# Kernel tuning notes

Hardware: AMD Instinct MI355X
Metric: run time of the kernel (lower is better)

The kernel has to match this reference:

```python
import jax, jax.numpy as jnp
import numpy as np

B, T, D, H = 2, 2048, 2048, 16
HD = D // H  # head_dim = 128
NEG = -1e9


def setup_inputs() -> dict:
    key = jax.random.key(0)
    k1, k2, k3 = jax.random.split(key, 3)
    x = jax.random.normal(k1, (B, T, D), dtype=jnp.float32)
    # additive causal mask: 0 on/below diagonal, large negative above
    mask = jnp.where(jnp.tril(jnp.ones((T, T), dtype=bool)), 0.0, NEG).astype(jnp.float32)
    causal_mask = mask[None, None]  # [1,1,T,T]
    w_qkv = jax.random.normal(k2, (3 * D, D), dtype=jnp.float32) * (D ** -0.5)
    w_out = jax.random.normal(k3, (D, D), dtype=jnp.float32) * (D ** -0.5)
    b_out = jnp.zeros((D,), dtype=jnp.float32)
    return {"x": x, "causal_mask": causal_mask, "w_qkv": w_qkv, "w_out": w_out, "b_out": b_out}


def reference(x, causal_mask, w_qkv, w_out, b_out):
    scale = HD ** -0.5
    qkv = jnp.einsum('btd,ed->bte', x, w_qkv)          # [B,T,3D]
    q, k, v = jnp.split(qkv, 3, axis=-1)
    def heads(t):  # [B,T,D] -> [B,H,T,HD]
        return t.reshape(B, T, H, HD).transpose(0, 2, 1, 3)
    q, k, v = heads(q), heads(k), heads(v)
    attn = jnp.einsum('bhqd,bhkd->bhqk', q, k) * scale + causal_mask
    attn = jax.nn.softmax(attn, axis=-1)
    out = jnp.einsum('bhqk,bhkd->bhqd', attn, v)       # [B,H,T,HD]
    out = out.transpose(0, 2, 1, 3).reshape(B, T, D)
    return jnp.einsum('btd,ed->bte', out, w_out) + b_out
```

## Files before the change

kernel.cpp:

```cpp
#include <hip/hip_runtime.h>
#include <stdint.h>

typedef uint16_t u16;
typedef __attribute__((ext_vector_type(8))) short short8;
typedef __attribute__((ext_vector_type(4))) float f32x4;
typedef __attribute__((ext_vector_type(16))) float f32x16;

#define MFMA16(a, b, c) __builtin_amdgcn_mfma_f32_16x16x32_bf16((a), (b), (c), 0, 0, 0)
#define MFMA32(a, b, c) __builtin_amdgcn_mfma_f32_32x32x16_bf16((a), (b), (c), 0, 0, 0)
#define AS1 __attribute__((address_space(1)))
#define AS3 __attribute__((address_space(3)))

__device__ __forceinline__ void gld_lds16(const u16* g, u16* l) {
  __builtin_amdgcn_global_load_lds((const AS1 void*)g, (AS3 void*)l, 16, 0, 0);
}

__device__ __forceinline__ u16 f2bf(float f) {
  uint32_t u = __float_as_uint(f);
  u += 0x7fffu + ((u >> 16) & 1u);
  return (u16)(u >> 16);
}

__global__ __launch_bounds__(256) void cvt_all(const float* __restrict__ x,
                                               const float* __restrict__ wqkv,
                                               const float* __restrict__ wout,
                                               u16* __restrict__ xb,
                                               u16* __restrict__ wqkvb,
                                               u16* __restrict__ woutb) {
  const int n1 = 8388608 / 4, n2 = 12582912 / 4;
  int i = blockIdx.x * 256 + threadIdx.x;
  const float* src;
  u16* dst;
  int j;
  if (i < n1) {
    src = x; dst = xb; j = i;
  } else if (i < n1 + n2) {
    src = wqkv; dst = wqkvb; j = i - n1;
  } else {
    src = wout; dst = woutb; j = i - n1 - n2;
  }
  float4 v = ((const float4*)src)[j];
  uint2 o;
  o.x = (uint32_t)f2bf(v.x) | ((uint32_t)f2bf(v.y) << 16);
  o.y = (uint32_t)f2bf(v.z) | ((uint32_t)f2bf(v.w) << 16);
  ((uint2*)dst)[j] = o;
}

__device__ __forceinline__ void gemm_core(const u16* __restrict__ Ab,
                                          const u16* __restrict__ Bb,
                                          int K, int lda, int ldb, u16* As,
                                          u16* Bs, int tid, f32x4 acc[4][4]) {
  const int lane = tid & 63, w = tid >> 6;
  const int wr = w >> 1, wc = w & 1;
  const int lo = lane & 15, q4 = lane >> 4;
  for (int k0 = 0; k0 < K; k0 += 64) {
#pragma unroll
    for (int s = 0; s < 4; ++s) {
      const int c = tid + s * 256;
      const int row = c >> 3, cc = c & 7;
      const int cs = cc ^ (row & 7);
      gld_lds16(Ab + (size_t)row * lda + k0 + cs * 8, As + c * 8);
      gld_lds16(Bb + (size_t)row * ldb + k0 + cs * 8, Bs + c * 8);
    }
    __syncthreads();
#pragma unroll
    for (int kk = 0; kk < 2; ++kk) {
      short8 af[4], bf[4];
#pragma unroll
      for (int i = 0; i < 4; ++i) {
        const int r = wr * 64 + i * 16 + lo;
        const int ch = (kk * 4 + q4) ^ (r & 7);
        af[i] = *(const short8*)(As + r * 64 + ch * 8);
      }
#pragma unroll
      for (int i = 0; i < 4; ++i) {
        const int r = wc * 64 + i * 16 + lo;
        const int ch = (kk * 4 + q4) ^ (r & 7);
        bf[i] = *(const short8*)(Bs + r * 64 + ch * 8);
      }
#pragma unroll
      for (int i = 0; i < 4; ++i)
#pragma unroll
        for (int j = 0; j < 4; ++j) acc[i][j] = MFMA16(af[i], bf[j], acc[i][j]);
    }
    __syncthreads();
  }
}

__global__ __launch_bounds__(256) void proj_gemm(const u16* __restrict__ xb,
                                                 const u16* __restrict__ wqkvb,
                                                 u16* __restrict__ qkb,
                                                 u16* __restrict__ vtb) {
  __shared__ u16 As[128 * 64];
  __shared__ u16 Bs[128 * 64];
  const int bx = blockIdx.x, tid = threadIdx.x;
  const u16 *Ab, *Bb;
  u16* C;
  if (bx < 1024) {
    const int mt = bx >> 5, nt = bx & 31;
    Ab = xb + (size_t)mt * 128 * 2048;
    Bb = wqkvb + (size_t)nt * 128 * 2048;
    C = qkb + (size_t)mt * 128 * 4096 + nt * 128;
  } else {
    const int idx = bx - 1024, mt = idx >> 5, nt = idx & 31;
    Ab = wqkvb + (size_t)(4096 + mt * 128) * 2048;
    Bb = xb + (size_t)nt * 128 * 2048;
    C = vtb + (size_t)mt * 128 * 4096 + nt * 128;
  }
  f32x4 acc[4][4];
  const f32x4 fzero = {0.f, 0.f, 0.f, 0.f};
#pragma unroll
  for (int i = 0; i < 4; ++i)
#pragma unroll
    for (int j = 0; j < 4; ++j) acc[i][j] = fzero;

  gemm_core(Ab, Bb, 2048, 2048, 2048, As, Bs, tid, acc);

  const int lane = tid & 63, w = tid >> 6;
  const int wr = w >> 1, wc = w & 1;
  const int lo = lane & 15, q4 = lane >> 4;
#pragma unroll
  for (int i = 0; i < 4; ++i)
#pragma unroll
    for (int j = 0; j < 4; ++j) {
      const int col = wc * 64 + j * 16 + lo;
#pragma unroll
      for (int e = 0; e < 4; ++e) {
        const int row = wr * 64 + i * 16 + q4 * 4 + e;
        C[(size_t)row * 4096 + col] = f2bf(acc[i][j][e]);
      }
    }
}

__global__ __launch_bounds__(256) void out_gemm(const u16* __restrict__ A,
                                                const u16* __restrict__ B,
                                                float* __restrict__ Cf,
                                                const float* __restrict__ bias) {
  __shared__ u16 As[128 * 64];
  __shared__ u16 Bs[128 * 64];
  const int bx = blockIdx.x, tid = threadIdx.x;
  const int mt = bx >> 4, nt = bx & 15;
  const u16* Ab = A + (size_t)mt * 128 * 2048;
  const u16* Bb = B + (size_t)nt * 128 * 2048;
  f32x4 acc[4][4];
  const f32x4 fzero = {0.f, 0.f, 0.f, 0.f};
#pragma unroll
  for (int i = 0; i < 4; ++i)
#pragma unroll
    for (int j = 0; j < 4; ++j) acc[i][j] = fzero;

  gemm_core(Ab, Bb, 2048, 2048, 2048, As, Bs, tid, acc);

  const int lane = tid & 63, w = tid >> 6;
  const int wr = w >> 1, wc = w & 1;
  const int lo = lane & 15, q4 = lane >> 4;
#pragma unroll
  for (int i = 0; i < 4; ++i)
#pragma unroll
    for (int j = 0; j < 4; ++j) {
      const int col = nt * 128 + wc * 64 + j * 16 + lo;
      const float bv = bias[col];
#pragma unroll
      for (int e = 0; e < 4; ++e) {
        const int row = mt * 128 + wr * 64 + i * 16 + q4 * 4 + e;
        Cf[(size_t)row * 2048 + col] = acc[i][j][e] + bv;
      }
    }
}

__device__ __forceinline__ int swz(int r, int c) {
  return r * 128 + (c ^ (((r ^ (r >> 3)) & 7) << 4));
}

__global__ __launch_bounds__(512) void flash_attn(const u16* __restrict__ qk,
                                                  const u16* __restrict__ vt,
                                                  u16* __restrict__ aout) {
  constexpr int T = 2048, WQK = 4096, D = 2048;
  constexpr int TILE = 128 * 128;
  __shared__ u16 smem[5 * TILE];

  const int bx = blockIdx.x;
  const int p = bx >> 5;
  const int g = bx & 31;
  const int h = g & 15, b = g >> 4;
  const int tid = threadIdx.x, lane = tid & 63, w = tid >> 6;
  const int wr = w >> 1, wcc = w & 1;
  const int l31 = lane & 31, h5 = lane >> 5;

  const u16* Qb = qk + (size_t)b * T * WQK + h * 128;
  const u16* Kb = Qb + 2048;
  const u16* Vtb = vt + (size_t)h * 128 * 4096 + b * 2048;
  u16* Ps = smem + 4 * TILE;

  const float cexp = 0.08838834764831843f * 1.4426950408889634f;
  short8 onesf;
#pragma unroll
  for (int j = 0; j < 8; ++j) onesf[j] = (short)0x3F80;

  for (int half = 0; half < 2; ++half) {
    const int qt = half ? p : 15 - p;
    const int q0 = qt * 128;

    short8 qf[8];
#pragma unroll
    for (int kc = 0; kc < 8; ++kc)
      qf[kc] = *(const short8*)(Qb + (size_t)(q0 + wr * 32 + l31) * WQK +
                                kc * 16 + h5 * 8);

    f32x16 o[2], osum;
#pragma unroll
    for (int e = 0; e < 16; ++e) { o[0][e] = 0.f; o[1][e] = 0.f; osum[e] = 0.f; }

    __syncthreads();
#pragma unroll
    for (int s = 0; s < 4; ++s) {
      const int c = tid + s * 512, r = c >> 4, cc = c & 15;
      const int cs = cc ^ (((r ^ (r >> 3)) & 7) << 1);
      gld_lds16(Kb + (size_t)r * WQK + cs * 8, smem + c * 8);
      gld_lds16(Vtb + (size_t)r * 4096 + cs * 8, smem + 2 * TILE + c * 8);
    }

    for (int kt = 0; kt <= qt; ++kt) {
      const int curo = (kt & 1) * TILE, nxto = TILE - curo;
      __syncthreads();
      if (kt < qt) {
        const int k0n = (kt + 1) * 128;
#pragma unroll
        for (int s = 0; s < 4; ++s) {
          const int c = tid + s * 512, r = c >> 4, cc = c & 15;
          const int cs = cc ^ (((r ^ (r >> 3)) & 7) << 1);
          gld_lds16(Kb + (size_t)(k0n + r) * WQK + cs * 8, smem + nxto + c * 8);
          gld_lds16(Vtb + (size_t)r * 4096 + k0n + cs * 8,
                    smem + 2 * TILE + nxto + c * 8);
        }
      }

      const u16* Ksc = smem + curo;
      const u16* Vsc = smem + 2 * TILE + curo;

      f32x16 s2[2];
#pragma unroll
      for (int e = 0; e < 16; ++e) { s2[0][e] = 0.f; s2[1][e] = 0.f; }
#pragma unroll
      for (int kc = 0; kc < 8; ++kc)
#pragma unroll
        for (int ct = 0; ct < 2; ++ct) {
          short8 kf = *(const short8*)&Ksc[swz(wcc * 64 + ct * 32 + l31,
                                               kc * 16 + h5 * 8)];
          s2[ct] = MFMA32(qf[kc], kf, s2[ct]);
        }

      const bool diag = (kt == qt);
#pragma unroll
      for (int ct = 0; ct < 2; ++ct) {
        const int kcol = wcc * 64 + ct * 32 + l31;
#pragma unroll
        for (int reg = 0; reg < 16; ++reg) {
          const int qrow = wr * 32 + (reg & 3) + 8 * (reg >> 2) + 4 * h5;
          float pv = exp2f(s2[ct][reg] * cexp);
          if (diag && (kcol > qrow)) pv = 0.f;
          Ps[swz(qrow, kcol)] = f2bf(pv);
        }
      }
      asm volatile("s_waitcnt lgkmcnt(0)\n\ts_barrier" ::: "memory");

#pragma unroll
      for (int kc = 0; kc < 8; ++kc) {
        short8 pa = *(const short8*)&Ps[swz(wr * 32 + l31, kc * 16 + h5 * 8)];
        osum = MFMA32(pa, onesf, osum);
#pragma unroll
        for (int dt = 0; dt < 2; ++dt) {
          short8 vf = *(const short8*)&Vsc[swz(wcc * 64 + dt * 32 + l31,
                                               kc * 16 + h5 * 8)];
          o[dt] = MFMA32(pa, vf, o[dt]);
        }
      }
    }

#pragma unroll
    for (int reg = 0; reg < 16; ++reg) {
      const int row = q0 + wr * 32 + (reg & 3) + 8 * (reg >> 2) + 4 * h5;
      const float inv = 1.f / osum[reg];
#pragma unroll
      for (int dt = 0; dt < 2; ++dt)
        aout[(size_t)(b * T + row) * D + h * 128 + wcc * 64 + dt * 32 + l31] =
            f2bf(o[dt][reg] * inv);
    }
  }
}

extern "C" void kernel_launch(void* const* d_in, const int* in_sizes, int n_in,
                              void* d_out, int out_size, void* d_ws, size_t ws_size,
                              hipStream_t stream) {
  const float* x = (const float*)d_in[0];
  const float* w_qkv = (const float*)d_in[2];
  const float* w_out = (const float*)d_in[3];
  const float* b_out = (const float*)d_in[4];
  float* out = (float*)d_out;

  const int BT = 4096, D = 2048, D3 = 6144;
  u16* xb = (u16*)d_ws;
  u16* wqkvb = xb + (size_t)BT * D;
  u16* woutb = wqkvb + (size_t)D3 * D;
  u16* qkb = woutb + (size_t)D * D;
  u16* vtb = qkb + (size_t)BT * 4096;
  u16* attnb = vtb + (size_t)D * BT;

  const int total4 = (BT * D + D3 * D + D * D) / 4;
  cvt_all<<<total4 / 256, 256, 0, stream>>>(x, w_qkv, w_out, xb, wqkvb, woutb);
  proj_gemm<<<1536, 256, 0, stream>>>(xb, wqkvb, qkb, vtb);
  flash_attn<<<256, 512, 0, stream>>>(qkb, vtb, attnb);
  out_gemm<<<512, 256, 0, stream>>>(attnb, woutb, out, b_out);
}
```

Measured before the change: 363.6 us.

## Triple-buffer GEMM K-loop with 256-row proj tiles and XCD-aware block remap

Replaces the single-buffered, two-barrier GEMM loop with a 3-stage LDS ring over K=32 slices. Each stage is issued two iterations ahead and guarded by one vmcnt-wait plus barrier, so global-to-LDS loads overlap the MFMAs. The projection GEMM moves to 256x128 tiles with 8 MFMA rows per wave, halving the grid, and both GEMMs remap block IDs so neighbouring tiles land on the same XCD for L2 reuse. The swizzle changes to a rotation, and MFMA sections are wrapped with s_setprio. The trade is more registers and LDS per block, which limits occupancy to 2 blocks per CU, plus more barriers per unit of work from the smaller K step.

```diff
diff --git a/kernel.cpp b/kernel.cpp
--- a/kernel.cpp
+++ b/kernel.cpp
@@ -46,99 +46,133 @@
   ((uint2*)dst)[j] = o;
 }
 
-__device__ __forceinline__ void gemm_core(const u16* __restrict__ Ab,
-                                          const u16* __restrict__ Bb,
-                                          int K, int lda, int ldb, u16* As,
-                                          u16* Bs, int tid, f32x4 acc[4][4]) {
+template <int N>
+__device__ __forceinline__ void bar_vm() {
+  asm volatile("s_waitcnt vmcnt(%0)\n\ts_barrier" ::"n"(N) : "memory");
+}
+
+template <int MFR>
+__device__ __forceinline__ void gemm_core3(const u16* __restrict__ Ab,
+                                           const u16* __restrict__ Bb,
+                                           u16* sm, int tid,
+                                           f32x4 acc[MFR][4]) {
+  constexpr int AROWS = MFR * 32;
+  constexpr int ASZ = AROWS * 32;
+  constexpr int BSZ = 128 * 32;
+  constexpr int BUF = ASZ + BSZ;
+  constexpr int NT = 64;
+  constexpr int ALD = AROWS / 64;
+  constexpr int VN = ALD + 2;
   const int lane = tid & 63, w = tid >> 6;
   const int wr = w >> 1, wc = w & 1;
   const int lo = lane & 15, q4 = lane >> 4;
-  for (int k0 = 0; k0 < K; k0 += 64) {
-#pragma unroll
-    for (int s = 0; s < 4; ++s) {
+  const int ch = (q4 + 4 - (lo >> 2)) & 3;
+
+  auto stage = [&](int g) {
+    u16* As = sm + (g % 3) * BUF;
+    u16* Bs = As + ASZ;
+    const int k0 = g * 32;
+#pragma unroll
+    for (int s = 0; s < ALD; ++s) {
       const int c = tid + s * 256;
-      const int row = c >> 3, cc = c & 7;
-      const int cs = cc ^ (row & 7);
-      gld_lds16(Ab + (size_t)row * lda + k0 + cs * 8, As + c * 8);
-      gld_lds16(Bb + (size_t)row * ldb + k0 + cs * 8, Bs + c * 8);
-    }
-    __syncthreads();
-#pragma unroll
-    for (int kk = 0; kk < 2; ++kk) {
-      short8 af[4], bf[4];
-#pragma unroll
-      for (int i = 0; i < 4; ++i) {
-        const int r = wr * 64 + i * 16 + lo;
-        const int ch = (kk * 4 + q4) ^ (r & 7);
-        af[i] = *(const short8*)(As + r * 64 + ch * 8);
-      }
-#pragma unroll
-      for (int i = 0; i < 4; ++i) {
-        const int r = wc * 64 + i * 16 + lo;
-        const int ch = (kk * 4 + q4) ^ (r & 7);
-        bf[i] = *(const short8*)(Bs + r * 64 + ch * 8);
-      }
-#pragma unroll
-      for (int i = 0; i < 4; ++i)
-#pragma unroll
-        for (int j = 0; j < 4; ++j) acc[i][j] = MFMA16(af[i], bf[j], acc[i][j]);
-    }
-    __syncthreads();
+      const int row = c >> 2, cc = c & 3;
+      const int cs = (cc + (row >> 2)) & 3;
+      gld_lds16(Ab + (size_t)row * 2048 + k0 + cs * 8, As + c * 8);
+    }
+#pragma unroll
+    for (int s = 0; s < 2; ++s) {
+      const int c = tid + s * 256;
+      const int row = c >> 2, cc = c & 3;
+      const int cs = (cc + (row >> 2)) & 3;
+      gld_lds16(Bb + (size_t)row * 2048 + k0 + cs * 8, Bs + c * 8);
+    }
+  };
+
+  stage(0);
+  stage(1);
+  bar_vm<VN>();
+
+  for (int g = 0; g < NT; ++g) {
+    const u16* As = sm + (g % 3) * BUF;
+    const u16* Bs = As + ASZ;
+    if (g + 2 < NT) stage(g + 2);
+    short8 af[MFR], bf[4];
+#pragma unroll
+    for (int i = 0; i < MFR; ++i)
+      af[i] = *(const short8*)(As + (wr * (MFR * 16) + i * 16 + lo) * 32 + ch * 8);
+#pragma unroll
+    for (int j = 0; j < 4; ++j)
+      bf[j] = *(const short8*)(Bs + (wc * 64 + j * 16 + lo) * 32 + ch * 8);
+    __builtin_amdgcn_s_setprio(1);
+#pragma unroll
+    for (int i = 0; i < MFR; ++i)
+#pragma unroll
+      for (int j = 0; j < 4; ++j) acc[i][j] = MFMA16(af[i], bf[j], acc[i][j]);
+    __builtin_amdgcn_s_setprio(0);
+    if (g + 1 < NT) {
+      if (g + 2 < NT) {
+        bar_vm<VN>();
+      } else {
+        bar_vm<0>();
+      }
+    }
   }
 }
 
-__global__ __launch_bounds__(256) void proj_gemm(const u16* __restrict__ xb,
-                                                 const u16* __restrict__ wqkvb,
-                                                 u16* __restrict__ qkb,
-                                                 u16* __restrict__ vtb) {
-  __shared__ u16 As[128 * 64];
-  __shared__ u16 Bs[128 * 64];
-  const int bx = blockIdx.x, tid = threadIdx.x;
+__global__ __launch_bounds__(256, 2) void proj_gemm(const u16* __restrict__ xb,
+                                                    const u16* __restrict__ wqkvb,
+                                                    u16* __restrict__ qkb,
+                                                    u16* __restrict__ vtb) {
+  __shared__ u16 sm[3 * (256 * 32 + 128 * 32)];
+  int bx = blockIdx.x;
+  bx = (bx & 7) * 96 + (bx >> 3);
+  const int tid = threadIdx.x;
   const u16 *Ab, *Bb;
   u16* C;
-  if (bx < 1024) {
+  if (bx < 512) {
     const int mt = bx >> 5, nt = bx & 31;
-    Ab = xb + (size_t)mt * 128 * 2048;
+    Ab = xb + (size_t)mt * 256 * 2048;
     Bb = wqkvb + (size_t)nt * 128 * 2048;
-    C = qkb + (size_t)mt * 128 * 4096 + nt * 128;
+    C = qkb + (size_t)mt * 256 * 4096 + nt * 128;
   } else {
-    const int idx = bx - 1024, mt = idx >> 5, nt = idx & 31;
-    Ab = wqkvb + (size_t)(4096 + mt * 128) * 2048;
+    const int idx = bx - 512, mt = idx >> 5, nt = idx & 31;
+    Ab = wqkvb + (size_t)(4096 + mt * 256) * 2048;
     Bb = xb + (size_t)nt * 128 * 2048;
-    C = vtb + (size_t)mt * 128 * 4096 + nt * 128;
+    C = vtb + (size_t)mt * 256 * 4096 + nt * 128;
   }
-  f32x4 acc[4][4];
+  f32x4 acc[8][4];
   const f32x4 fzero = {0.f, 0.f, 0.f, 0.f};
 #pragma unroll
-  for (int i = 0; i < 4; ++i)
+  for (int i = 0; i < 8; ++i)
 #pragma unroll
     for (int j = 0; j < 4; ++j) acc[i][j] = fzero;
 
-  gemm_core(Ab, Bb, 2048, 2048, 2048, As, Bs, tid, acc);
+  gemm_core3<8>(Ab, Bb, sm, tid, acc);
 
   const int lane = tid & 63, w = tid >> 6;
   const int wr = w >> 1, wc = w & 1;
   const int lo = lane & 15, q4 = lane >> 4;
 #pragma unroll
-  for (int i = 0; i < 4; ++i)
+  for (int i = 0; i < 8; ++i)
 #pragma unroll
     for (int j = 0; j < 4; ++j) {
       const int col = wc * 64 + j * 16 + lo;
 #pragma unroll
       for (int e = 0; e < 4; ++e) {
-        const int row = wr * 64 + i * 16 + q4 * 4 + e;
+        const int row = wr * 128 + i * 16 + q4 * 4 + e;
         C[(size_t)row * 4096 + col] = f2bf(acc[i][j][e]);
       }
     }
 }
 
-__global__ __launch_bounds__(256) void out_gemm(const u16* __restrict__ A,
-                                                const u16* __restrict__ B,
-                                                float* __restrict__ Cf,
-                                                const float* __restrict__ bias) {
-  __shared__ u16 As[128 * 64];
-  __shared__ u16 Bs[128 * 64];
-  const int bx = blockIdx.x, tid = threadIdx.x;
+__global__ __launch_bounds__(256, 2) void out_gemm(const u16* __restrict__ A,
+                                                   const u16* __restrict__ B,
+                                                   float* __restrict__ Cf,
+                                                   const float* __restrict__ bias) {
+  __shared__ u16 sm[3 * (128 * 32 + 128 * 32)];
+  int bx = blockIdx.x;
+  bx = (bx & 7) * 64 + (bx >> 3);
+  const int tid = threadIdx.x;
   const int mt = bx >> 4, nt = bx & 15;
   const u16* Ab = A + (size_t)mt * 128 * 2048;
   const u16* Bb = B + (size_t)nt * 128 * 2048;
@@ -149,7 +183,7 @@
 #pragma unroll
     for (int j = 0; j < 4; ++j) acc[i][j] = fzero;
 
-  gemm_core(Ab, Bb, 2048, 2048, 2048, As, Bs, tid, acc);
+  gemm_core3<4>(Ab, Bb, sm, tid, acc);
 
   const int lane = tid & 63, w = tid >> 6;
   const int wr = w >> 1, wc = w & 1;
@@ -308,7 +342,7 @@
 
   const int total4 = (BT * D + D3 * D + D * D) / 4;
   cvt_all<<<total4 / 256, 256, 0, stream>>>(x, w_qkv, w_out, xb, wqkvb, woutb);
-  proj_gemm<<<1536, 256, 0, stream>>>(xb, wqkvb, qkb, vtb);
+  proj_gemm<<<768, 256, 0, stream>>>(xb, wqkvb, qkb, vtb);
   flash_attn<<<256, 512, 0, stream>>>(qkb, vtb, attnb);
   out_gemm<<<512, 256, 0, stream>>>(attnb, woutb, out, b_out);
 }
```

Result: no change. 357.6 us (-1.6%).
